# Kernel tuning notes

Hardware: AMD Instinct MI355X
Metric: run time of the kernel (lower is better)

The kernel has to match this reference:

```python
import jax, jax.numpy as jnp
import numpy as np

EPS = 1e-10


def _gcn(X, A, W, act):
    # A_hat = A + I; symmetric normalization D^{-1/2} A_hat D^{-1/2}
    N = A.shape[0]
    A_hat = A + jnp.eye(N, dtype=A.dtype)
    d = 1.0 / jnp.sqrt(jnp.sum(A_hat, axis=1) + EPS)
    A_norm = (d[:, None] * A_hat) * d[None, :]  # same math as diag @ A_hat @ diag
    return act(A_norm @ (X @ W))


def _pool(X, A, s, k):
    scores = (X @ s)[:, 0]            # [N]
    _, idx = jax.lax.top_k(scores, k)  # static k (ceil(ratio*N))
    return X[idx], A[idx][:, idx], idx


def _unpool(Xp, idx, N):
    return jnp.zeros((N, Xp.shape[-1]), Xp.dtype).at[idx].set(Xp)


def _glorot(key, shape):
    lim = np.sqrt(6.0 / (shape[0] + shape[1])).astype(np.float32)
    return jax.random.uniform(key, shape, jnp.float32, -lim, lim)


def setup_inputs() -> dict:
    key = jax.random.key(0)
    ks = jax.random.split(key, 8)
    N, F_IN, F, C = 8192, 16, 32, 2
    x = jax.random.normal(ks[0], (N, F_IN), jnp.float32)
    # sparse-ish symmetric binary adjacency stored densely (as the module expects)
    a = (jax.random.uniform(ks[1], (N, N)) < 0.01).astype(jnp.float32)
    a = jnp.maximum(a, a.T)
    return {
        "x": x,
        "a": a,
        "W1": _glorot(ks[2], (F_IN, F)),
        "W2": _glorot(ks[3], (F, F)),
        "W3": _glorot(ks[4], (F, F)),
        "W4": _glorot(ks[5], (F, C)),
        "s1": _glorot(ks[6], (F, 1)),
        "s2": _glorot(ks[7], (F, 1)),
    }


def reference(x, a, W1, W2, W3, W4, s1, s2):
    N = x.shape[0]
    K1 = int(np.ceil(0.5 * N))   # pool1 ratio 0.5
    K2 = int(np.ceil(0.5 * K1))  # pool2 ratio 0.5
    relu = jax.nn.relu
    X1 = _gcn(x, a, W1, relu)                     # [N, F]
    X1p, A1p, idx1 = _pool(X1, a, s1, K1)         # [K1, F], [K1, K1]
    X2 = _gcn(X1p, A1p, W2, relu)                 # [K1, F]
    X2p, _, idx2 = _pool(X2, A1p, s2, K2)         # [K2, F]
    X3 = _unpool(X2p, idx2, K1)                   # scatter back to [K1, F]
    X3 = _gcn(X3, A1p, W3, relu)
    X4 = _unpool(X3, idx1, N)                     # scatter back to [N, F]
    return _gcn(X4, a, W4, lambda z: jax.nn.softmax(z, axis=-1))
```

## Files before the change

### kernel.cpp

```cpp
#include <hip/hip_runtime.h>
#include <stdint.h>

#define NNODES 8192
#define KP1 4096
#define KP2 2048
#define FIN 16
#define FH 32
#define COUT 2
#define STRA 320
#define STRS 320

__global__ __launch_bounds__(256) void build_ell(const float* __restrict__ A, int n, int stride,
        int* __restrict__ ell, int* __restrict__ rowcnt, int* __restrict__ diag, float* __restrict__ dnorm)
{
    __shared__ int cnt;
    __shared__ int dg;
    int row = blockIdx.x;
    if (threadIdx.x == 0) { cnt = 0; dg = 0; }
    __syncthreads();
    const float4* arow4 = (const float4*)(A + (size_t)row * n);
    int* erow = ell + (size_t)row * stride;
    int n4 = n >> 2;
    for (int c4 = threadIdx.x; c4 < n4; c4 += 256) {
        float4 v = arow4[c4];
        int cb = c4 << 2;
        if (v.x != 0.0f) {
            if (cb == row) dg = 1;
            else { int p = atomicAdd(&cnt, 1); if (p < stride) erow[p] = cb; }
        }
        if (v.y != 0.0f) {
            int c = cb + 1;
            if (c == row) dg = 1;
            else { int p = atomicAdd(&cnt, 1); if (p < stride) erow[p] = c; }
        }
        if (v.z != 0.0f) {
            int c = cb + 2;
            if (c == row) dg = 1;
            else { int p = atomicAdd(&cnt, 1); if (p < stride) erow[p] = c; }
        }
        if (v.w != 0.0f) {
            int c = cb + 3;
            if (c == row) dg = 1;
            else { int p = atomicAdd(&cnt, 1); if (p < stride) erow[p] = c; }
        }
    }
    __syncthreads();
    if (threadIdx.x == 0) {
        int cf = cnt;
        rowcnt[row] = cf < stride ? cf : stride;
        diag[row] = dg;
        dnorm[row] = rsqrtf((float)(cf + dg + 1) + 1e-10f);
    }
}

__global__ __launch_bounds__(256) void feat_gemm(const float* __restrict__ X, const int* __restrict__ gather,
        const int* __restrict__ mask, const float* __restrict__ W, float* __restrict__ Z,
        int n, int kdim, int fout)
{
    int t = blockIdx.x * 256 + threadIdx.x;
    int i = t / fout;
    int f = t - i * fout;
    if (i >= n) return;
    int j = i;
    if (gather) j = gather[i];
    int ok = (j >= 0);
    if (mask && mask[i] < 0) ok = 0;
    float acc = 0.0f;
    if (ok) {
        const float* xr = X + (size_t)j * kdim;
        for (int k = 0; k < kdim; ++k) acc += xr[k] * W[k * fout + f];
    }
    Z[(size_t)i * fout + f] = acc;
}

__global__ __launch_bounds__(256) void spmm_f32(const int* __restrict__ ell, const int* __restrict__ rowcnt,
        const int* __restrict__ diag, const float* __restrict__ dnorm, const float* __restrict__ Z,
        const int* __restrict__ remap, const int* __restrict__ maskp,
        float* __restrict__ X, float* __restrict__ scores, const float* __restrict__ svec,
        int n, int stride)
{
    int wid = (blockIdx.x * 256 + threadIdx.x) >> 6;
    int lane = threadIdx.x & 63;
    if (wid >= n) return;
    int g = lane >> 3;
    int q = lane & 7;
    int cnt = rowcnt[wid];
    const int* erow = ell + (size_t)wid * stride;
    float ax = 0.0f, ay = 0.0f, az = 0.0f, aw = 0.0f;
    for (int it = g; it < cnt; it += 8) {
        int c = erow[it];
        if (maskp && maskp[c] < 0) continue;
        int zc = c;
        if (remap) zc = remap[c];
        float dn = dnorm[c];
        const float4* zp = (const float4*)(Z + (size_t)zc * 32);
        float4 zv = zp[q];
        ax += dn * zv.x;
        ay += dn * zv.y;
        az += dn * zv.z;
        aw += dn * zv.w;
    }
    ax += __shfl_xor(ax, 8);
    ay += __shfl_xor(ay, 8);
    az += __shfl_xor(az, 8);
    aw += __shfl_xor(aw, 8);
    ax += __shfl_xor(ax, 16);
    ay += __shfl_xor(ay, 16);
    az += __shfl_xor(az, 16);
    aw += __shfl_xor(aw, 16);
    ax += __shfl_xor(ax, 32);
    ay += __shfl_xor(ay, 32);
    az += __shfl_xor(az, 32);
    aw += __shfl_xor(aw, 32);
    if (g == 0) {
        float dr = dnorm[wid];
        int selfok = 1;
        if (maskp && maskp[wid] < 0) selfok = 0;
        if (selfok) {
            int zc = wid;
            if (remap) zc = remap[wid];
            const float4* zp = (const float4*)(Z + (size_t)zc * 32);
            float4 zv = zp[q];
            float cf = (float)(diag[wid] + 1) * dr;
            ax += cf * zv.x;
            ay += cf * zv.y;
            az += cf * zv.z;
            aw += cf * zv.w;
        }
        float4 o;
        o.x = fmaxf(dr * ax, 0.0f);
        o.y = fmaxf(dr * ay, 0.0f);
        o.z = fmaxf(dr * az, 0.0f);
        o.w = fmaxf(dr * aw, 0.0f);
        float4* xp = (float4*)(X + (size_t)wid * 32);
        xp[q] = o;
        if (scores) {
            const float4* sp = (const float4*)svec;
            float4 sv = sp[q];
            float p = o.x * sv.x + o.y * sv.y + o.z * sv.z + o.w * sv.w;
            p += __shfl_xor(p, 1);
            p += __shfl_xor(p, 2);
            p += __shfl_xor(p, 4);
            if (q == 0) scores[wid] = p;
        }
    }
}

__global__ __launch_bounds__(256) void spmm_out(const int* __restrict__ ell, const int* __restrict__ rowcnt,
        const int* __restrict__ diag, const float* __restrict__ dnorm, const float* __restrict__ Z,
        float* __restrict__ out, int n, int stride)
{
    int wid = (blockIdx.x * 256 + threadIdx.x) >> 6;
    int lane = threadIdx.x & 63;
    if (wid >= n) return;
    int cnt = rowcnt[wid];
    const int* erow = ell + (size_t)wid * stride;
    const float2* Z2 = (const float2*)Z;
    float ax = 0.0f, ay = 0.0f;
    for (int it = lane; it < cnt; it += 64) {
        int c = erow[it];
        float dn = dnorm[c];
        float2 zv = Z2[c];
        ax += dn * zv.x;
        ay += dn * zv.y;
    }
    ax += __shfl_xor(ax, 1);
    ay += __shfl_xor(ay, 1);
    ax += __shfl_xor(ax, 2);
    ay += __shfl_xor(ay, 2);
    ax += __shfl_xor(ax, 4);
    ay += __shfl_xor(ay, 4);
    ax += __shfl_xor(ax, 8);
    ay += __shfl_xor(ay, 8);
    ax += __shfl_xor(ax, 16);
    ay += __shfl_xor(ay, 16);
    ax += __shfl_xor(ax, 32);
    ay += __shfl_xor(ay, 32);
    if (lane == 0) {
        float dr = dnorm[wid];
        float cf = (float)(diag[wid] + 1) * dr;
        float2 zs = Z2[wid];
        ax += cf * zs.x;
        ay += cf * zs.y;
        float v0 = dr * ax;
        float v1 = dr * ay;
        float m = fmaxf(v0, v1);
        float e0 = __expf(v0 - m);
        float e1 = __expf(v1 - m);
        float inv = 1.0f / (e0 + e1);
        float2 r;
        r.x = e0 * inv;
        r.y = e1 * inv;
        ((float2*)out)[wid] = r;
    }
}

__global__ __launch_bounds__(256) void topk_select(const float* __restrict__ scores, int n, int K,
        int* __restrict__ rank, int* __restrict__ idxlist)
{
    __shared__ unsigned int km_s[8192];
    __shared__ unsigned int part_s[256];
    __shared__ unsigned int histp[4][256];
    __shared__ unsigned int sh_pref;
    __shared__ unsigned int sh_rem;
    int tid = threadIdx.x;
    int wv = tid >> 6;
    int per = n >> 8;
    int base = tid * per;
    for (int e = 0; e < per; ++e) {
        int v = base + e;
        unsigned int u = __float_as_uint(scores[v]);
        unsigned int m;
        if (u & 0x80000000u) m = ~u; else m = u | 0x80000000u;
        km_s[v] = ~m;
    }
    if (tid == 0) { sh_pref = 0u; sh_rem = (unsigned int)K; }
    __syncthreads();
    for (int bp = 3; bp >= 0; --bp) {
        histp[0][tid] = 0u;
        histp[1][tid] = 0u;
        histp[2][tid] = 0u;
        histp[3][tid] = 0u;
        __syncthreads();
        unsigned int maskhi = 0u;
        if (bp < 3) maskhi = 0xFFFFFFFFu << ((bp + 1) * 8);
        unsigned int pref = sh_pref;
        unsigned int rem = sh_rem;
        for (int e = 0; e < per; ++e) {
            unsigned int km = km_s[base + e];
            if ((km & maskhi) == pref) atomicAdd(&histp[wv][(km >> (bp * 8)) & 255u], 1u);
        }
        __syncthreads();
        unsigned int tot = histp[0][tid] + histp[1][tid] + histp[2][tid] + histp[3][tid];
        part_s[tid] = tot;
        __syncthreads();
        for (int offd = 1; offd < 256; offd <<= 1) {
            unsigned int add = 0u;
            if (tid >= offd) add = part_s[tid - offd];
            __syncthreads();
            part_s[tid] += add;
            __syncthreads();
        }
        unsigned int cum = part_s[tid];
        if (tot != 0u && cum >= rem && cum - tot < rem) {
            sh_pref = pref | ((unsigned int)tid << (bp * 8));
            sh_rem = rem - (cum - tot);
        }
        __syncthreads();
    }
    unsigned int T = sh_pref;
    unsigned int need_eq = sh_rem;
    unsigned int run = 0u;
    for (int e = 0; e < per; ++e) {
        unsigned int km = km_s[base + e];
        if (km < T) run += 0x10000u;
        else if (km == T) run += 1u;
    }
    part_s[tid] = run;
    __syncthreads();
    for (int offd = 1; offd < 256; offd <<= 1) {
        unsigned int add = 0u;
        if (tid >= offd) add = part_s[tid - offd];
        __syncthreads();
        part_s[tid] += add;
        __syncthreads();
    }
    unsigned int cur = part_s[tid] - run;
    for (int e = 0; e < per; ++e) {
        int v = base + e;
        unsigned int km = km_s[v];
        unsigned int ltb = cur >> 16;
        unsigned int eqb = cur & 0xFFFFu;
        unsigned int eqs = eqb < need_eq ? eqb : need_eq;
        int sel = 0;
        if (km < T) { sel = 1; cur += 0x10000u; }
        else if (km == T) { if (eqb < need_eq) sel = 1; cur += 1u; }
        if (sel) {
            int r = (int)(ltb + eqs);
            rank[v] = r;
            idxlist[r] = v;
        } else {
            rank[v] = -1;
        }
    }
}

__global__ __launch_bounds__(256) void build_subell(const int* __restrict__ ellA, const int* __restrict__ rowcntA,
        const int* __restrict__ diagA, const int* __restrict__ idx1, const int* __restrict__ rank1,
        int* __restrict__ ellS, int* __restrict__ rowcntS, int* __restrict__ diagS, float* __restrict__ dnormS,
        int k1, int strideA, int strideS)
{
    int wid = (blockIdx.x * 256 + threadIdx.x) >> 6;
    int lane = threadIdx.x & 63;
    if (wid >= k1) return;
    int r = idx1[wid];
    int cnt = rowcntA[r];
    const int* erow = ellA + (size_t)r * strideA;
    int* srow = ellS + (size_t)wid * strideS;
    int outn = 0;
    for (int t0 = 0; t0 < cnt; t0 += 64) {
        int it = t0 + lane;
        int rk = -1;
        if (it < cnt) rk = rank1[erow[it]];
        unsigned long long b = __ballot(rk >= 0);
        int ofs = __popcll(b & ((1ull << lane) - 1ull));
        if (rk >= 0) srow[outn + ofs] = rk;
        outn += __popcll(b);
    }
    if (lane == 0) {
        int dg = diagA[r];
        rowcntS[wid] = outn;
        diagS[wid] = dg;
        dnormS[wid] = rsqrtf((float)(outn + dg + 1) + 1e-10f);
    }
}

#define CARVE(type, name, bytes) \
    type name = (type)wp; wp += (((size_t)(bytes)) + 255) & ~((size_t)255);

extern "C" void kernel_launch(void* const* d_in, const int* in_sizes, int n_in,
                              void* d_out, int out_size, void* d_ws, size_t ws_size,
                              hipStream_t stream)
{
    const float* x  = (const float*)d_in[0];
    const float* a  = (const float*)d_in[1];
    const float* W1 = (const float*)d_in[2];
    const float* W2 = (const float*)d_in[3];
    const float* W3 = (const float*)d_in[4];
    const float* W4 = (const float*)d_in[5];
    const float* s1 = (const float*)d_in[6];
    const float* s2 = (const float*)d_in[7];
    float* out = (float*)d_out;
    (void)in_sizes; (void)n_in; (void)out_size; (void)ws_size;

    char* wp = (char*)d_ws;
    CARVE(int*,   ellA,  (size_t)NNODES * STRA * sizeof(int));
    CARVE(int*,   cntA,  NNODES * sizeof(int));
    CARVE(int*,   diagA, NNODES * sizeof(int));
    CARVE(float*, dnA,   NNODES * sizeof(float));
    CARVE(float*, Z1,    (size_t)NNODES * FH * sizeof(float));
    CARVE(float*, X1,    (size_t)NNODES * FH * sizeof(float));
    CARVE(float*, sc1,   NNODES * sizeof(float));
    CARVE(int*,   rank1, NNODES * sizeof(int));
    CARVE(int*,   idx1,  NNODES * sizeof(int));
    CARVE(int*,   ellS,  (size_t)KP1 * STRS * sizeof(int));
    CARVE(int*,   cntS,  KP1 * sizeof(int));
    CARVE(int*,   diagS, KP1 * sizeof(int));
    CARVE(float*, dnS,   KP1 * sizeof(float));
    CARVE(float*, Z2,    (size_t)KP1 * FH * sizeof(float));
    CARVE(float*, X2,    (size_t)KP1 * FH * sizeof(float));
    CARVE(float*, sc2,   KP1 * sizeof(float));
    CARVE(int*,   rank2, KP1 * sizeof(int));
    CARVE(int*,   idx2,  KP1 * sizeof(int));
    CARVE(float*, Z3,    (size_t)KP1 * FH * sizeof(float));
    CARVE(float*, X3g,   (size_t)KP1 * FH * sizeof(float));
    CARVE(float*, Z4,    (size_t)NNODES * COUT * sizeof(float));

    build_ell<<<NNODES, 256, 0, stream>>>(a, NNODES, STRA, ellA, cntA, diagA, dnA);
    feat_gemm<<<(NNODES * FH) / 256, 256, 0, stream>>>(x, (const int*)0, (const int*)0, W1, Z1, NNODES, FIN, FH);
    spmm_f32<<<NNODES / 4, 256, 0, stream>>>(ellA, cntA, diagA, dnA, Z1,
        (const int*)0, (const int*)0, X1, sc1, s1, NNODES, STRA);
    topk_select<<<1, 256, 0, stream>>>(sc1, NNODES, KP1, rank1, idx1);
    build_subell<<<KP1 / 4, 256, 0, stream>>>(ellA, cntA, diagA, idx1, rank1, ellS, cntS, diagS, dnS, KP1, STRA, STRS);
    feat_gemm<<<(KP1 * FH) / 256, 256, 0, stream>>>(X1, idx1, (const int*)0, W2, Z2, KP1, FH, FH);
    spmm_f32<<<KP1 / 4, 256, 0, stream>>>(ellS, cntS, diagS, dnS, Z2,
        (const int*)0, (const int*)0, X2, sc2, s2, KP1, STRS);
    topk_select<<<1, 256, 0, stream>>>(sc2, KP1, KP2, rank2, idx2);
    feat_gemm<<<(KP1 * FH) / 256, 256, 0, stream>>>(X2, (const int*)0, rank2, W3, Z3, KP1, FH, FH);
    spmm_f32<<<KP1 / 4, 256, 0, stream>>>(ellS, cntS, diagS, dnS, Z3,
        (const int*)0, rank2, X3g, (float*)0, (const float*)0, KP1, STRS);
    feat_gemm<<<(NNODES * COUT) / 256, 256, 0, stream>>>(X3g, rank1, (const int*)0, W4, Z4, NNODES, FH, COUT);
    spmm_out<<<NNODES / 4, 256, 0, stream>>>(ellA, cntA, diagA, dnA, Z4, out, NNODES, STRA);
}
```

Before: 506.8 us.

## Scan upper-triangle adjacency with symmetric insert and fuse feature GEMMs into neighbouring kernels

The dense adjacency scan now reads only the upper triangle and inserts each edge into both rows with global atomics, roughly halving the dense read. Degree finalisation moves to a small separate kernel. Feature GEMMs are folded into idle blocks of the build and top-k kernels (computed for all nodes, then gathered through remap), and the W4 projection is fused into the third SpMM epilogue. This cuts kernel launches and dense traffic, but neighbour order in the ELL rows becomes nondeterministic and more atomics hit global memory.

```diff
diff --git a/kernel.cpp b/kernel.cpp
--- a/kernel.cpp
+++ b/kernel.cpp
@@ -10,73 +10,96 @@
 #define STRA 320
 #define STRS 320
 
-__global__ __launch_bounds__(256) void build_ell(const float* __restrict__ A, int n, int stride,
-        int* __restrict__ ell, int* __restrict__ rowcnt, int* __restrict__ diag, float* __restrict__ dnorm)
-{
-    __shared__ int cnt;
+__global__ __launch_bounds__(256) void zero_cnt(int* __restrict__ c, int n)
+{
+    int i = blockIdx.x * 256 + threadIdx.x;
+    if (i < n) c[i] = 0;
+}
+
+__global__ __launch_bounds__(256) void build_sym(const float* __restrict__ A, int n, int stride,
+        int* __restrict__ ell, int* __restrict__ gcnt, int* __restrict__ diag,
+        const float* __restrict__ Xf, const float* __restrict__ Wf, float* __restrict__ Zf, int kf)
+{
+    if ((int)blockIdx.x >= n) {
+        int t = ((int)blockIdx.x - n) * 256 + threadIdx.x;
+        int i = t >> 5;
+        int f = t & 31;
+        const float* xr = Xf + (size_t)i * kf;
+        float acc = 0.0f;
+        for (int k = 0; k < kf; ++k) acc += xr[k] * Wf[k * 32 + f];
+        Zf[t] = acc;
+        return;
+    }
     __shared__ int dg;
     int row = blockIdx.x;
-    if (threadIdx.x == 0) { cnt = 0; dg = 0; }
+    if (threadIdx.x == 0) dg = 0;
     __syncthreads();
     const float4* arow4 = (const float4*)(A + (size_t)row * n);
-    int* erow = ell + (size_t)row * stride;
     int n4 = n >> 2;
-    for (int c4 = threadIdx.x; c4 < n4; c4 += 256) {
+    int s4 = row >> 2;
+    for (int c4 = s4 + threadIdx.x; c4 < n4; c4 += 256) {
         float4 v = arow4[c4];
         int cb = c4 << 2;
         if (v.x != 0.0f) {
-            if (cb == row) dg = 1;
-            else { int p = atomicAdd(&cnt, 1); if (p < stride) erow[p] = cb; }
+            int c = cb;
+            if (c == row) dg = 1;
+            else if (c > row) {
+                int p = atomicAdd(&gcnt[row], 1);
+                if (p < stride) ell[(size_t)row * stride + p] = c;
+                int q = atomicAdd(&gcnt[c], 1);
+                if (q < stride) ell[(size_t)c * stride + q] = row;
+            }
         }
         if (v.y != 0.0f) {
             int c = cb + 1;
             if (c == row) dg = 1;
-            else { int p = atomicAdd(&cnt, 1); if (p < stride) erow[p] = c; }
+            else if (c > row) {
+                int p = atomicAdd(&gcnt[row], 1);
+                if (p < stride) ell[(size_t)row * stride + p] = c;
+                int q = atomicAdd(&gcnt[c], 1);
+                if (q < stride) ell[(size_t)c * stride + q] = row;
+            }
         }
         if (v.z != 0.0f) {
             int c = cb + 2;
             if (c == row) dg = 1;
-            else { int p = atomicAdd(&cnt, 1); if (p < stride) erow[p] = c; }
+            else if (c > row) {
+                int p = atomicAdd(&gcnt[row], 1);
+                if (p < stride) ell[(size_t)row * stride + p] = c;
+                int q = atomicAdd(&gcnt[c], 1);
+                if (q < stride) ell[(size_t)c * stride + q] = row;
+            }
         }
         if (v.w != 0.0f) {
             int c = cb + 3;
             if (c == row) dg = 1;
-            else { int p = atomicAdd(&cnt, 1); if (p < stride) erow[p] = c; }
+            else if (c > row) {
+                int p = atomicAdd(&gcnt[row], 1);
+                if (p < stride) ell[(size_t)row * stride + p] = c;
+                int q = atomicAdd(&gcnt[c], 1);
+                if (q < stride) ell[(size_t)c * stride + q] = row;
+            }
         }
     }
     __syncthreads();
-    if (threadIdx.x == 0) {
-        int cf = cnt;
-        rowcnt[row] = cf < stride ? cf : stride;
-        diag[row] = dg;
-        dnorm[row] = rsqrtf((float)(cf + dg + 1) + 1e-10f);
-    }
-}
-
-__global__ __launch_bounds__(256) void feat_gemm(const float* __restrict__ X, const int* __restrict__ gather,
-        const int* __restrict__ mask, const float* __restrict__ W, float* __restrict__ Z,
-        int n, int kdim, int fout)
-{
-    int t = blockIdx.x * 256 + threadIdx.x;
-    int i = t / fout;
-    int f = t - i * fout;
+    if (threadIdx.x == 0) diag[row] = dg;
+}
+
+__global__ __launch_bounds__(256) void finalize_deg(const int* __restrict__ gcnt, const int* __restrict__ diag,
+        int* __restrict__ rowcnt, float* __restrict__ dnorm, int n, int stride)
+{
+    int i = blockIdx.x * 256 + threadIdx.x;
     if (i >= n) return;
-    int j = i;
-    if (gather) j = gather[i];
-    int ok = (j >= 0);
-    if (mask && mask[i] < 0) ok = 0;
-    float acc = 0.0f;
-    if (ok) {
-        const float* xr = X + (size_t)j * kdim;
-        for (int k = 0; k < kdim; ++k) acc += xr[k] * W[k * fout + f];
-    }
-    Z[(size_t)i * fout + f] = acc;
+    int c = gcnt[i];
+    rowcnt[i] = c < stride ? c : stride;
+    dnorm[i] = rsqrtf((float)(c + diag[i] + 1) + 1e-10f);
 }
 
 __global__ __launch_bounds__(256) void spmm_f32(const int* __restrict__ ell, const int* __restrict__ rowcnt,
         const int* __restrict__ diag, const float* __restrict__ dnorm, const float* __restrict__ Z,
         const int* __restrict__ remap, const int* __restrict__ maskp,
         float* __restrict__ X, float* __restrict__ scores, const float* __restrict__ svec,
+        const float* __restrict__ W4p, float* __restrict__ z4out,
         int n, int stride)
 {
     int wid = (blockIdx.x * 256 + threadIdx.x) >> 6;
@@ -127,42 +150,66 @@
             az += cf * zv.z;
             aw += cf * zv.w;
         }
-        float4 o;
-        o.x = fmaxf(dr * ax, 0.0f);
-        o.y = fmaxf(dr * ay, 0.0f);
-        o.z = fmaxf(dr * az, 0.0f);
-        o.w = fmaxf(dr * aw, 0.0f);
-        float4* xp = (float4*)(X + (size_t)wid * 32);
-        xp[q] = o;
-        if (scores) {
-            const float4* sp = (const float4*)svec;
-            float4 sv = sp[q];
-            float p = o.x * sv.x + o.y * sv.y + o.z * sv.z + o.w * sv.w;
-            p += __shfl_xor(p, 1);
-            p += __shfl_xor(p, 2);
-            p += __shfl_xor(p, 4);
-            if (q == 0) scores[wid] = p;
+        float ox = fmaxf(dr * ax, 0.0f);
+        float oy = fmaxf(dr * ay, 0.0f);
+        float oz = fmaxf(dr * az, 0.0f);
+        float ow = fmaxf(dr * aw, 0.0f);
+        if (z4out) {
+            int kb = q * 4;
+            float p0 = ox * W4p[(kb + 0) * 2 + 0] + oy * W4p[(kb + 1) * 2 + 0]
+                     + oz * W4p[(kb + 2) * 2 + 0] + ow * W4p[(kb + 3) * 2 + 0];
+            float p1 = ox * W4p[(kb + 0) * 2 + 1] + oy * W4p[(kb + 1) * 2 + 1]
+                     + oz * W4p[(kb + 2) * 2 + 1] + ow * W4p[(kb + 3) * 2 + 1];
+            p0 += __shfl_xor(p0, 1);
+            p1 += __shfl_xor(p1, 1);
+            p0 += __shfl_xor(p0, 2);
+            p1 += __shfl_xor(p1, 2);
+            p0 += __shfl_xor(p0, 4);
+            p1 += __shfl_xor(p1, 4);
+            if (q == 0) {
+                float2 r;
+                r.x = p0;
+                r.y = p1;
+                ((float2*)z4out)[wid] = r;
+            }
+        } else {
+            float4 o;
+            o.x = ox; o.y = oy; o.z = oz; o.w = ow;
+            float4* xp = (float4*)(X + (size_t)wid * 32);
+            xp[q] = o;
+            if (scores) {
+                const float4* sp = (const float4*)svec;
+                float4 sv = sp[q];
+                float p = o.x * sv.x + o.y * sv.y + o.z * sv.z + o.w * sv.w;
+                p += __shfl_xor(p, 1);
+                p += __shfl_xor(p, 2);
+                p += __shfl_xor(p, 4);
+                if (q == 0) scores[wid] = p;
+            }
         }
     }
 }
 
 __global__ __launch_bounds__(256) void spmm_out(const int* __restrict__ ell, const int* __restrict__ rowcnt,
-        const int* __restrict__ diag, const float* __restrict__ dnorm, const float* __restrict__ Z,
-        float* __restrict__ out, int n, int stride)
+        const int* __restrict__ diag, const float* __restrict__ dnorm, const float* __restrict__ Zr,
+        const int* __restrict__ gat, float* __restrict__ out, int n, int stride)
 {
     int wid = (blockIdx.x * 256 + threadIdx.x) >> 6;
     int lane = threadIdx.x & 63;
     if (wid >= n) return;
     int cnt = rowcnt[wid];
     const int* erow = ell + (size_t)wid * stride;
-    const float2* Z2 = (const float2*)Z;
+    const float2* Z2 = (const float2*)Zr;
     float ax = 0.0f, ay = 0.0f;
     for (int it = lane; it < cnt; it += 64) {
         int c = erow[it];
-        float dn = dnorm[c];
-        float2 zv = Z2[c];
-        ax += dn * zv.x;
-        ay += dn * zv.y;
+        int rk = gat[c];
+        if (rk >= 0) {
+            float dn = dnorm[c];
+            float2 zv = Z2[rk];
+            ax += dn * zv.x;
+            ay += dn * zv.y;
+        }
     }
     ax += __shfl_xor(ax, 1);
     ay += __shfl_xor(ay, 1);
@@ -178,10 +225,13 @@
     ay += __shfl_xor(ay, 32);
     if (lane == 0) {
         float dr = dnorm[wid];
-        float cf = (float)(diag[wid] + 1) * dr;
-        float2 zs = Z2[wid];
-        ax += cf * zs.x;
-        ay += cf * zs.y;
+        int rks = gat[wid];
+        if (rks >= 0) {
+            float cf = (float)(diag[wid] + 1) * dr;
+            float2 zs = Z2[rks];
+            ax += cf * zs.x;
+            ay += cf * zs.y;
+        }
         float v0 = dr * ax;
         float v1 = dr * ay;
         float m = fmaxf(v0, v1);
@@ -195,9 +245,20 @@
     }
 }
 
-__global__ __launch_bounds__(256) void topk_select(const float* __restrict__ scores, int n, int K,
-        int* __restrict__ rank, int* __restrict__ idxlist)
-{
+__global__ __launch_bounds__(256) void topk_feat(const float* __restrict__ scores, int n, int K,
+        int* __restrict__ rank, int* __restrict__ idxlist,
+        const float* __restrict__ Xf, const float* __restrict__ Wf, float* __restrict__ Zf, int kf)
+{
+    if (blockIdx.x != 0) {
+        int t = ((int)blockIdx.x - 1) * 256 + threadIdx.x;
+        int i = t >> 5;
+        int f = t & 31;
+        const float* xr = Xf + (size_t)i * kf;
+        float acc = 0.0f;
+        for (int k = 0; k < kf; ++k) acc += xr[k] * Wf[k * 32 + f];
+        Zf[t] = acc;
+        return;
+    }
     __shared__ unsigned int km_s[8192];
     __shared__ unsigned int part_s[256];
     __shared__ unsigned int histp[4][256];
@@ -335,6 +396,7 @@
 
     char* wp = (char*)d_ws;
     CARVE(int*,   ellA,  (size_t)NNODES * STRA * sizeof(int));
+    CARVE(int*,   gcntA, NNODES * sizeof(int));
     CARVE(int*,   cntA,  NNODES * sizeof(int));
     CARVE(int*,   diagA, NNODES * sizeof(int));
     CARVE(float*, dnA,   NNODES * sizeof(float));
@@ -347,28 +409,29 @@
     CARVE(int*,   cntS,  KP1 * sizeof(int));
     CARVE(int*,   diagS, KP1 * sizeof(int));
     CARVE(float*, dnS,   KP1 * sizeof(float));
-    CARVE(float*, Z2,    (size_t)KP1 * FH * sizeof(float));
+    CARVE(float*, Z2f,   (size_t)NNODES * FH * sizeof(float));
     CARVE(float*, X2,    (size_t)KP1 * FH * sizeof(float));
     CARVE(float*, sc2,   KP1 * sizeof(float));
     CARVE(int*,   rank2, KP1 * sizeof(int));
     CARVE(int*,   idx2,  KP1 * sizeof(int));
-    CARVE(float*, Z3,    (size_t)KP1 * FH * sizeof(float));
-    CARVE(float*, X3g,   (size_t)KP1 * FH * sizeof(float));
-    CARVE(float*, Z4,    (size_t)NNODES * COUT * sizeof(float));
-
-    build_ell<<<NNODES, 256, 0, stream>>>(a, NNODES, STRA, ellA, cntA, diagA, dnA);
-    feat_gemm<<<(NNODES * FH) / 256, 256, 0, stream>>>(x, (const int*)0, (const int*)0, W1, Z1, NNODES, FIN, FH);
+    CARVE(float*, Z3f,   (size_t)KP1 * FH * sizeof(float));
+    CARVE(float*, Z4r,   (size_t)KP1 * COUT * sizeof(float));
+
+    zero_cnt<<<NNODES / 256, 256, 0, stream>>>(gcntA, NNODES);
+    build_sym<<<NNODES + (NNODES * FH) / 256, 256, 0, stream>>>(
+        a, NNODES, STRA, ellA, gcntA, diagA, x, W1, Z1, FIN);
+    finalize_deg<<<NNODES / 256, 256, 0, stream>>>(gcntA, diagA, cntA, dnA, NNODES, STRA);
     spmm_f32<<<NNODES / 4, 256, 0, stream>>>(ellA, cntA, diagA, dnA, Z1,
-        (const int*)0, (const int*)0, X1, sc1, s1, NNODES, STRA);
-    topk_select<<<1, 256, 0, stream>>>(sc1, NNODES, KP1, rank1, idx1);
-    build_subell<<<KP1 / 4, 256, 0, stream>>>(ellA, cntA, diagA, idx1, rank1, ellS, cntS, diagS, dnS, KP1, STRA, STRS);
-    feat_gemm<<<(KP1 * FH) / 256, 256, 0, stream>>>(X1, idx1, (const int*)0, W2, Z2, KP1, FH, FH);
-    spmm_f32<<<KP1 / 4, 256, 0, stream>>>(ellS, cntS, diagS, dnS, Z2,
-        (const int*)0, (const int*)0, X2, sc2, s2, KP1, STRS);
-    topk_select<<<1, 256, 0, stream>>>(sc2, KP1, KP2, rank2, idx2);
-    feat_gemm<<<(KP1 * FH) / 256, 256, 0, stream>>>(X2, (const int*)0, rank2, W3, Z3, KP1, FH, FH);
-    spmm_f32<<<KP1 / 4, 256, 0, stream>>>(ellS, cntS, diagS, dnS, Z3,
-        (const int*)0, rank2, X3g, (float*)0, (const float*)0, KP1, STRS);
-    feat_gemm<<<(NNODES * COUT) / 256, 256, 0, stream>>>(X3g, rank1, (const int*)0, W4, Z4, NNODES, FH, COUT);
-    spmm_out<<<NNODES / 4, 256, 0, stream>>>(ellA, cntA, diagA, dnA, Z4, out, NNODES, STRA);
-}
+        (const int*)0, (const int*)0, X1, sc1, s1, (const float*)0, (float*)0, NNODES, STRA);
+    topk_feat<<<1 + (NNODES * FH) / 256, 256, 0, stream>>>(
+        sc1, NNODES, KP1, rank1, idx1, X1, W2, Z2f, FH);
+    build_subell<<<KP1 / 4, 256, 0, stream>>>(ellA, cntA, diagA, idx1, rank1,
+        ellS, cntS, diagS, dnS, KP1, STRA, STRS);
+    spmm_f32<<<KP1 / 4, 256, 0, stream>>>(ellS, cntS, diagS, dnS, Z2f,
+        idx1, (const int*)0, X2, sc2, s2, (const float*)0, (float*)0, KP1, STRS);
+    topk_feat<<<1 + (KP1 * FH) / 256, 256, 0, stream>>>(
+        sc2, KP1, KP2, rank2, idx2, X2, W3, Z3f, FH);
+    spmm_f32<<<KP1 / 4, 256, 0, stream>>>(ellS, cntS, diagS, dnS, Z3f,
+        (const int*)0, rank2, (float*)0, (float*)0, (const float*)0, W4, Z4r, KP1, STRS);
+    spmm_out<<<NNODES / 4, 256, 0, stream>>>(ellA, cntA, diagA, dnA, Z4r, rank1, out, NNODES, STRA);
+}
```

After: 523.4 us. 1.03x slower.
